# Performance work log

Measured on AMD Instinct MI355X. Metric: run time of the kernel, lower is better.

Reference implementation:

```python
import math
import jax, jax.numpy as jnp
import numpy as np

B, T, C = 4, 8192, 1024
EPS = 1e-5
LAYER_ID, N_LAYERS = 0, 24


def setup_inputs() -> dict:
    key = jax.random.key(0)
    ks = jax.random.split(key, 6)
    x = jax.random.normal(ks[0], (B, T, C), dtype=jnp.float32)
    # time_decay / time_first initialized exactly as in the torch __init__
    ratio_1_to_almost0 = 1.0 - LAYER_ID / N_LAYERS
    h = np.arange(C, dtype=np.float64)
    time_decay = (-5.0 + 8.0 * (h / (C - 1)) ** (0.7 + 1.3 * ratio_1_to_almost0)).astype(np.float32)
    zigzag = (((np.arange(C) + 1) % 3) - 1).astype(np.float32) * 0.5
    time_first = (math.log(0.3) + zigzag).astype(np.float32)
    # nn.Linear(dim, dim, bias=False) weights, stored as (out, in)
    std = 0.02
    Wk = jax.random.normal(ks[1], (C, C), dtype=jnp.float32) * std
    Wv = jax.random.normal(ks[2], (C, C), dtype=jnp.float32) * std
    Wr = jax.random.normal(ks[3], (C, C), dtype=jnp.float32) * std
    Wo = jax.random.normal(ks[4], (C, C), dtype=jnp.float32) * std
    ln_w = jnp.ones((C,), dtype=jnp.float32)
    ln_b = jnp.zeros((C,), dtype=jnp.float32)
    return {
        "x": x,
        "time_decay": jnp.asarray(time_decay),
        "time_first": jnp.asarray(time_first),
        "Wk": Wk, "Wv": Wv, "Wr": Wr, "Wo": Wo,
        "ln_w": ln_w, "ln_b": ln_b,
    }


def reference(x, time_decay, time_first, Wk, Wv, Wr, Wo, ln_w, ln_b):
    # LayerNorm (ln_x)
    mu = jnp.mean(x, axis=-1, keepdims=True)
    var = jnp.mean(jnp.square(x - mu), axis=-1, keepdims=True)
    xx = (x - mu) * jax.lax.rsqrt(var + EPS) * ln_w + ln_b

    # k, v, r projections (nn.Linear: y = x @ W^T)
    k = jnp.einsum('btc,dc->btd', xx, Wk)
    v = jnp.einsum('btc,dc->btd', xx, Wv)
    r = jnp.einsum('btc,dc->btd', xx, Wr)

    td = -jnp.exp(time_decay)   # (C,)
    tf = jnp.exp(time_first)    # (C,)

    # In the original loop, position j is weighted exp(td * j) regardless of t,
    # so wkv_history[t] = sum_{j < t} exp(td*j) * k[j] * v[j]  (exclusive cumsum).
    tpos = jnp.arange(T, dtype=jnp.float32)[:, None]        # (T,1)
    w = jnp.exp(td[None, :] * tpos)                         # (T,C)
    kv = k * v * w[None]                                    # (B,T,C)
    hist = jnp.cumsum(kv, axis=1) - kv                      # exclusive cumsum
    wkv = hist + k * tf

    out = jax.nn.sigmoid(r) * wkv
    return jnp.einsum('btc,dc->btd', out, Wo)
```

## Files before the change

kernel.cpp:

```cpp
#include <hip/hip_runtime.h>
#include <stdint.h>

#define B_ 4
#define T_ 8192
#define C_ 1024
#define BT_ (B_*T_)
#define NSEG 64
#define SLEN (T_/NSEG)
#define EPS_ 1e-5f
#define NT_ 16

typedef __attribute__((ext_vector_type(8))) short short8;
typedef __attribute__((ext_vector_type(4))) float float4v;
typedef __attribute__((ext_vector_type(4))) unsigned short ushort4v;
typedef unsigned short u16;

__device__ __forceinline__ u16 f2bf(float f){
  union { float f; uint32_t u; } v; v.f = f;
  uint32_t r = v.u + 0x7FFFu + ((v.u >> 16) & 1u);
  return (u16)(r >> 16);
}
__device__ __forceinline__ float bf2f(u16 h){
  union { uint32_t u; float f; } v; v.u = ((uint32_t)h) << 16;
  return v.f;
}
__device__ __forceinline__ void gload16(const void* g, void* l){
  __builtin_amdgcn_global_load_lds((__attribute__((address_space(1))) void*)(void*)g,
                                   (__attribute__((address_space(3))) void*)l,
                                   16, 0, 0);
}

__global__ void castw_kernel(const float* __restrict__ in, u16* __restrict__ out){
  int i = blockIdx.x*blockDim.x + threadIdx.x;
  float4v v = ((const float4v*)in)[i];
  ushort4v o;
  o.x=f2bf(v.x); o.y=f2bf(v.y); o.z=f2bf(v.z); o.w=f2bf(v.w);
  ((ushort4v*)out)[i] = o;
}

__global__ __launch_bounds__(256) void ln_kernel(const float* __restrict__ x,
    const float* __restrict__ lw, const float* __restrict__ lb, u16* __restrict__ xxb)
{
  int row = blockIdx.x;
  int tid = threadIdx.x;
  float4v v = ((const float4v*)(x + (size_t)row*C_))[tid];
  float s1 = v.x+v.y+v.z+v.w;
  float s2 = v.x*v.x+v.y*v.y+v.z*v.z+v.w*v.w;
  #pragma unroll
  for (int off=32; off>0; off>>=1){
    s1 += __shfl_down(s1, off, 64);
    s2 += __shfl_down(s2, off, 64);
  }
  __shared__ float red1[4], red2[4];
  if ((tid&63)==0){ red1[tid>>6]=s1; red2[tid>>6]=s2; }
  __syncthreads();
  s1 = red1[0]+red1[1]+red1[2]+red1[3];
  s2 = red2[0]+red2[1]+red2[2]+red2[3];
  float mu = s1*(1.0f/C_);
  float rs = rsqrtf(s2*(1.0f/C_) - mu*mu + EPS_);
  float4v wv = ((const float4v*)lw)[tid];
  float4v bv = ((const float4v*)lb)[tid];
  ushort4v o;
  o.x = f2bf((v.x-mu)*rs*wv.x + bv.x);
  o.y = f2bf((v.y-mu)*rs*wv.y + bv.y);
  o.z = f2bf((v.z-mu)*rs*wv.z + bv.z);
  o.w = f2bf((v.w-mu)*rs*wv.w + bv.w);
  ((ushort4v*)(xxb + (size_t)row*C_))[tid] = o;
}

#define SYNC() do{ __builtin_amdgcn_sched_barrier(0); __builtin_amdgcn_s_barrier(); __builtin_amdgcn_sched_barrier(0); }while(0)

#define RD_A(DST, MH, BO) \
  _Pragma("unroll") for (int mt=0; mt<4; ++mt) \
    _Pragma("unroll") for (int ks=0; ks<2; ++ks) \
      DST[mt*2+ks] = *(const short8*)(lds + (BO) + ks*16384 + aoff0 + ((MH)*4+mt)*1024);

#define RD_B(DST, NH, BO) \
  _Pragma("unroll") for (int nt=0; nt<2; ++nt) \
    _Pragma("unroll") for (int ks=0; ks<2; ++ks) \
      DST[nt*2+ks] = *(const short8*)(lds + (BO) + ks*16384 + boff0 + ((NH)*2+nt)*1024);

#define MFMA_Q(AS, BS, MH, NH) do{ \
  __builtin_amdgcn_s_setprio(1); \
  _Pragma("unroll") for (int ks=0; ks<2; ++ks) \
    _Pragma("unroll") for (int mt=0; mt<4; ++mt) \
      _Pragma("unroll") for (int nt=0; nt<2; ++nt) \
        acc[(MH)*4+mt][(NH)*2+nt] = __builtin_amdgcn_mfma_f32_16x16x32_bf16( \
            AS[mt*2+ks], BS[nt*2+ks], acc[(MH)*4+mt][(NH)*2+nt], 0,0,0); \
  __builtin_amdgcn_s_setprio(0); \
}while(0)

template<bool F32OUT>
__global__ __launch_bounds__(512, 2) void gemm_dp(const u16* __restrict__ A,
    const u16* __restrict__ Bw, void* __restrict__ C0, void* __restrict__ C1,
    void* __restrict__ C2, int nbn)
{
  __shared__ __align__(1024) char lds[131072];

  const int tid  = threadIdx.x;
  const int lane = tid & 63;
  const int wid  = tid >> 6;
  const int wr   = wid >> 2;
  const int wc   = wid & 3;

  const int lin = blockIdx.x;
  const int x   = lin & 7;
  const int wl  = lin >> 3;
  const int bm  = x*16 + wl / nbn;
  const int bn  = wl % nbn;

  const int l15   = lane & 15;
  const int lswz  = ((lane>>4) ^ ((l15>>1)&3)) << 4;
  const int aoff0 = (wr*128 + l15)*64 + lswz;
  const int boff0 = 65536 + (wc*64 + l15)*64 + lswz;

  const int kk   = wid >> 2;
  const int rg0  = (wid & 3)*2;
  const int kkL  = kk*16384;
  const char* Asrc = ((const char*)A)  + ((size_t)bm*256 + (lane>>2))*2048
                     + (((lane&3) ^ ((lane>>3)&3)) << 4) + kk*64;
  const char* Bsrc = ((const char*)Bw) + ((size_t)bn*256 + (lane>>2))*2048
                     + (((lane&3) ^ ((lane>>3)&3)) << 4) + kk*64;

  float4v acc[8][4];
  float4v zero = {0.f,0.f,0.f,0.f};
  #pragma unroll
  for (int i=0;i<8;++i)
    #pragma unroll
    for (int j=0;j<4;++j) acc[i][j]=zero;

  auto stage = [&](int bo, int ktB){
    #pragma unroll
    for (int h=0; h<2; ++h)
      #pragma unroll
      for (int q=0; q<2; ++q){
        const int rowoff = h*128 + (rg0+q)*16;
        gload16(Asrc + (size_t)rowoff*2048 + ktB, lds + bo + kkL + rowoff*64);
        gload16(Bsrc + (size_t)rowoff*2048 + ktB, lds + 65536 + bo + kkL + rowoff*64);
      }
  };

  stage(0, 0);
  stage(32768, 128);
  asm volatile("s_waitcnt vmcnt(8)" ::: "memory");
  SYNC();

  short8 A0r[8], A1r[8], B0r[4], B1r[4];

  #define KTILE(KT, BO) do{ \
     \
    RD_A(A0r, 0, BO); RD_B(B0r, 0, BO); \
    SYNC(); \
    MFMA_Q(A0r, B0r, 0, 0); \
    SYNC(); \
     \
    RD_A(A1r, 1, BO); \
    SYNC(); \
    MFMA_Q(A1r, B0r, 1, 0); \
    SYNC(); \
     \
    RD_B(B1r, 1, BO); \
    SYNC(); \
    MFMA_Q(A1r, B1r, 1, 1); \
    SYNC(); \
     \
    if ((KT) < NT_-2) stage(BO, ((KT)+2)*128); \
    MFMA_Q(A0r, B1r, 0, 1); \
    if ((KT) < NT_-1){ \
      if ((KT) < NT_-2) { asm volatile("s_waitcnt vmcnt(8)" ::: "memory"); } \
      else              { asm volatile("s_waitcnt vmcnt(0)" ::: "memory"); } \
      SYNC(); \
    } \
  }while(0)

  for (int kt2=0; kt2<NT_; kt2+=2){
    KTILE(kt2,   0);
    KTILE(kt2+1, 32768);
  }
  #undef KTILE

  const int cl = l15, rq = lane >> 4;
  const size_t rbase = (size_t)bm*256 + wr*128;
  const int sel = bn >> 2;
  const int c0 = (bn&3)*256 + wc*64;
  void* cb = (sel==0) ? C0 : ((sel==1) ? C1 : C2);
  #pragma unroll
  for (int mi=0;mi<8;++mi)
    #pragma unroll
    for (int ni=0;ni<4;++ni)
      #pragma unroll
      for (int j=0;j<4;++j){
        size_t rr = rbase + mi*16 + rq*4 + j;
        int    cc = c0 + ni*16 + cl;
        if constexpr (F32OUT) ((float*)cb)[rr*1024 + cc] = acc[mi][ni][j];
        else                  ((u16*)cb)[rr*1024 + cc]   = f2bf(acc[mi][ni][j]);
      }
}

__global__ __launch_bounds__(256) void wkv_pass1(const u16* __restrict__ kb,
    const u16* __restrict__ vb, const float* __restrict__ tdecay,
    float* __restrict__ segsum)
{
  int c   = blockIdx.x*256 + threadIdx.x;
  int seg = blockIdx.y, b = blockIdx.z;
  float td = -expf(tdecay[c]);
  float d  = expf(td);
  int t0   = seg*SLEN;
  float w  = expf(td * (float)t0);
  size_t base = ((size_t)b*T_ + t0)*C_ + c;
  float s = 0.f;
  for (int i=0;i<SLEN;++i){
    float kk = bf2f(kb[base + (size_t)i*C_]);
    float vv = bf2f(vb[base + (size_t)i*C_]);
    s += kk*vv*w;
    w *= d;
  }
  segsum[((size_t)b*NSEG + seg)*C_ + c] = s;
}

__global__ void wkv_pass2(const float* __restrict__ segsum, float* __restrict__ segoff){
  int idx = blockIdx.x*256 + threadIdx.x;
  int b = idx / C_, c = idx % C_;
  float run = 0.f;
  for (int s=0;s<NSEG;++s){
    size_t o = ((size_t)b*NSEG + s)*C_ + c;
    segoff[o] = run;
    run += segsum[o];
  }
}

__global__ __launch_bounds__(256) void wkv_pass3(const u16* __restrict__ kb,
    const u16* __restrict__ vb, const u16* __restrict__ rb,
    const float* __restrict__ tdecay, const float* __restrict__ tfirst,
    const float* __restrict__ segoff, u16* __restrict__ outb)
{
  int c   = blockIdx.x*256 + threadIdx.x;
  int seg = blockIdx.y, b = blockIdx.z;
  float td = -expf(tdecay[c]);
  float d  = expf(td);
  float tf = expf(tfirst[c]);
  int t0   = seg*SLEN;
  float w  = expf(td * (float)t0);
  float hist = segoff[((size_t)b*NSEG + seg)*C_ + c];
  size_t base = ((size_t)b*T_ + t0)*C_ + c;
  for (int i=0;i<SLEN;++i){
    float kk = bf2f(kb[base + (size_t)i*C_]);
    float vv = bf2f(vb[base + (size_t)i*C_]);
    float rr = bf2f(rb[base + (size_t)i*C_]);
    float wkv = hist + kk*tf;
    float sg  = 1.f/(1.f + expf(-rr));
    outb[base + (size_t)i*C_] = f2bf(sg*wkv);
    hist += kk*vv*w;
    w *= d;
  }
}

extern "C" void kernel_launch(void* const* d_in, const int* in_sizes, int n_in,
                              void* d_out, int out_size, void* d_ws, size_t ws_size,
                              hipStream_t stream)
{
  (void)in_sizes; (void)n_in; (void)out_size; (void)ws_size;
  const float* x   = (const float*)d_in[0];
  const float* tdc = (const float*)d_in[1];
  const float* tfc = (const float*)d_in[2];
  const float* Wk  = (const float*)d_in[3];
  const float* Wv  = (const float*)d_in[4];
  const float* Wr  = (const float*)d_in[5];
  const float* Wo  = (const float*)d_in[6];
  const float* lw  = (const float*)d_in[7];
  const float* lb  = (const float*)d_in[8];
  float* out = (float*)d_out;

  char* ws = (char*)d_ws;
  u16* xxb = (u16*)(ws);
  u16* rb  = (u16*)(ws + 67108864);
  u16* Wkb = (u16*)(ws + 134217728);
  u16* Wvb = (u16*)(ws + 136314880);
  u16* Wrb = (u16*)(ws + 138412032);
  u16* Wob = (u16*)(ws + 140509184);
  float* segsum = (float*)(ws + 142606336);
  float* segoff = (float*)(ws + 143654912);
  u16* kb = (u16*)d_out;
  u16* vb = kb + (size_t)BT_*C_;
  u16* outb = xxb;

  castw_kernel<<<1024,256,0,stream>>>(Wk, Wkb);
  castw_kernel<<<1024,256,0,stream>>>(Wv, Wvb);
  castw_kernel<<<1024,256,0,stream>>>(Wr, Wrb);
  castw_kernel<<<1024,256,0,stream>>>(Wo, Wob);

  ln_kernel<<<BT_,256,0,stream>>>(x, lw, lb, xxb);

  gemm_dp<false><<<1536,512,0,stream>>>(xxb, Wkb, kb, vb, rb, 12);

  dim3 sg(C_/256, NSEG, B_);
  wkv_pass1<<<sg,256,0,stream>>>(kb, vb, tdc, segsum);
  wkv_pass2<<<16,256,0,stream>>>(segsum, segoff);
  wkv_pass3<<<sg,256,0,stream>>>(kb, vb, rb, tdc, tfc, segoff, outb);

  gemm_dp<true><<<512,512,0,stream>>>(outb, Wob, out, out, out, 4);
}
```

Measured before the change: 500.2 us.

## Software-pipeline LDS fragment reads across k-tiles and merge weight casts

The GEMM inner loop now double-buffers the first A/B register fragments: the next tile's fragments are read from the other LDS buffer while the current MFMAs run. Sched barriers pin that interleaving and one of the SYNCs between quarter-steps is dropped. The global-load wait changes from vmcnt(8) to vmcnt(0) earlier in each tile, which may expose more load latency. Separately, the four weight-cast launches are merged into one 2D-grid launch to cut launch overhead.

Result: slower. 883.0 us (+76.5%).

```diff
diff --git a/kernel.cpp b/kernel.cpp
--- a/kernel.cpp
+++ b/kernel.cpp
@@ -30,9 +30,13 @@
                                    16, 0, 0);
 }
 
-__global__ void castw_kernel(const float* __restrict__ in, u16* __restrict__ out){
+__global__ void castw4_kernel(const float* __restrict__ s0, const float* __restrict__ s1,
+                              const float* __restrict__ s2, const float* __restrict__ s3,
+                              u16* __restrict__ dst){
+  const float* src = (blockIdx.y==0)?s0:((blockIdx.y==1)?s1:((blockIdx.y==2)?s2:s3));
+  u16* out = dst + (size_t)blockIdx.y*1048576;
   int i = blockIdx.x*blockDim.x + threadIdx.x;
-  float4v v = ((const float4v*)in)[i];
+  float4v v = ((const float4v*)src)[i];
   ushort4v o;
   o.x=f2bf(v.x); o.y=f2bf(v.y); o.z=f2bf(v.z); o.w=f2bf(v.w);
   ((ushort4v*)out)[i] = o;
@@ -145,39 +149,38 @@
   asm volatile("s_waitcnt vmcnt(8)" ::: "memory");
   SYNC();
 
-  short8 A0r[8], A1r[8], B0r[4], B1r[4];
-
-  #define KTILE(KT, BO) do{ \
-     \
-    RD_A(A0r, 0, BO); RD_B(B0r, 0, BO); \
-    SYNC(); \
-    MFMA_Q(A0r, B0r, 0, 0); \
-    SYNC(); \
+  short8 A0e[8], A0o[8], A1r[8], B0e[4], B0o[4], B1r[4];
+  RD_A(A0e, 0, 0); RD_B(B0e, 0, 0);
+
+  #define TILE(KT, BO, A0c, B0c, A0n, B0n) do{ \
      \
     RD_A(A1r, 1, BO); \
-    SYNC(); \
-    MFMA_Q(A1r, B0r, 1, 0); \
+    __builtin_amdgcn_sched_barrier(0); \
+    MFMA_Q(A0c, B0c, 0, 0); \
     SYNC(); \
      \
     RD_B(B1r, 1, BO); \
+    __builtin_amdgcn_sched_barrier(0); \
+    MFMA_Q(A1r, B0c, 1, 0); \
+    asm volatile("s_waitcnt vmcnt(0)" ::: "memory"); \
     SYNC(); \
+     \
+    if ((KT) < NT_-1){ RD_A(A0n, 0, (BO)^32768); RD_B(B0n, 0, (BO)^32768); } \
+    __builtin_amdgcn_sched_barrier(0); \
     MFMA_Q(A1r, B1r, 1, 1); \
     SYNC(); \
      \
     if ((KT) < NT_-2) stage(BO, ((KT)+2)*128); \
-    MFMA_Q(A0r, B1r, 0, 1); \
-    if ((KT) < NT_-1){ \
-      if ((KT) < NT_-2) { asm volatile("s_waitcnt vmcnt(8)" ::: "memory"); } \
-      else              { asm volatile("s_waitcnt vmcnt(0)" ::: "memory"); } \
-      SYNC(); \
-    } \
+    __builtin_amdgcn_sched_barrier(0); \
+    MFMA_Q(A0c, B1r, 0, 1); \
+    SYNC(); \
   }while(0)
 
   for (int kt2=0; kt2<NT_; kt2+=2){
-    KTILE(kt2,   0);
-    KTILE(kt2+1, 32768);
-  }
-  #undef KTILE
+    TILE(kt2,   0,     A0e, B0e, A0o, B0o);
+    TILE(kt2+1, 32768, A0o, B0o, A0e, B0e);
+  }
+  #undef TILE
 
   const int cl = l15, rq = lane >> 4;
   const size_t rbase = (size_t)bm*256 + wr*128;
@@ -275,19 +278,14 @@
   u16* xxb = (u16*)(ws);
   u16* rb  = (u16*)(ws + 67108864);
   u16* Wkb = (u16*)(ws + 134217728);
-  u16* Wvb = (u16*)(ws + 136314880);
-  u16* Wrb = (u16*)(ws + 138412032);
-  u16* Wob = (u16*)(ws + 140509184);
   float* segsum = (float*)(ws + 142606336);
   float* segoff = (float*)(ws + 143654912);
   u16* kb = (u16*)d_out;
   u16* vb = kb + (size_t)BT_*C_;
   u16* outb = xxb;
-
-  castw_kernel<<<1024,256,0,stream>>>(Wk, Wkb);
-  castw_kernel<<<1024,256,0,stream>>>(Wv, Wvb);
-  castw_kernel<<<1024,256,0,stream>>>(Wr, Wrb);
-  castw_kernel<<<1024,256,0,stream>>>(Wo, Wob);
+  u16* Wob = Wkb + 3u*1048576u;
+
+  castw4_kernel<<<dim3(1024,4),256,0,stream>>>(Wk, Wv, Wr, Wo, Wkb);
 
   ln_kernel<<<BT_,256,0,stream>>>(x, lw, lb, xxb);
 
```
